# Kernel tuning notes

Measured on AMD Instinct MI355X. Metric: run time of the kernel, lower is better.

The kernel has to match this reference:

```python
import jax, jax.numpy as jnp
import numpy as np

EMBED_DIM = 1536
NUM_HEADS = 12
HEAD_DIM = EMBED_DIM // NUM_HEADS  # 128
SEQ = 2048
EPS = 1e-5


def rms_norm(x, w):
    # x: (..., HEAD_DIM)
    var = jnp.mean(jnp.square(x), axis=-1, keepdims=True)
    return x * jax.lax.rsqrt(var + EPS) * w


def apply_rotary(x, cos, sin):
    # x: (b, s, h, d); cos/sin: (s, d/2) -> broadcast (1, s, 1, d/2)
    d2 = cos.shape[-1]
    c = cos[None, :, None, :]
    s_ = sin[None, :, None, :]
    x1, x2 = x[..., :d2], x[..., d2:]
    return jnp.concatenate([x1 * c - x2 * s_, x2 * c + x1 * s_], axis=-1)


def setup_inputs() -> dict:
    key = jax.random.key(0)
    ks = jax.random.split(key, 10)
    x = jax.random.normal(ks[0], (SEQ, 1, EMBED_DIM), dtype=jnp.float32)
    cu_seqlens = jnp.array([0, SEQ // 2, SEQ], dtype=jnp.int32)
    # rotary tables for positions 0..SEQ-1, rotary dim = HEAD_DIM
    inv_freq = 1.0 / (10000.0 ** (jnp.arange(0, HEAD_DIM, 2, dtype=jnp.float32) / HEAD_DIM))
    pos = jnp.arange(SEQ, dtype=jnp.float32)
    freqs = pos[:, None] * inv_freq[None, :]  # (s, d/2)
    rotary_pos_emb_cos = jnp.cos(freqs)
    rotary_pos_emb_sin = jnp.sin(freqs)
    scale = 0.02
    w_qkv = jax.random.normal(ks[1], (EMBED_DIM, 3 * EMBED_DIM), dtype=jnp.float32) * scale
    b_qkv = jnp.zeros((3 * EMBED_DIM,), dtype=jnp.float32)
    q_norm_w = jnp.ones((HEAD_DIM,), dtype=jnp.float32)
    k_norm_w = jnp.ones((HEAD_DIM,), dtype=jnp.float32)
    w_proj = jax.random.normal(ks[2], (EMBED_DIM, EMBED_DIM), dtype=jnp.float32) * scale
    b_proj = jnp.zeros((EMBED_DIM,), dtype=jnp.float32)
    return {
        'x': x, 'cu_seqlens': cu_seqlens,
        'rotary_pos_emb_cos': rotary_pos_emb_cos, 'rotary_pos_emb_sin': rotary_pos_emb_sin,
        'w_qkv': w_qkv, 'b_qkv': b_qkv, 'q_norm_w': q_norm_w, 'k_norm_w': k_norm_w,
        'w_proj': w_proj, 'b_proj': b_proj,
    }


def reference(x, cu_seqlens, rotary_pos_emb_cos, rotary_pos_emb_sin,
              w_qkv, b_qkv, q_norm_w, k_norm_w, w_proj, b_proj):
    s, b, e = x.shape
    h, d = NUM_HEADS, HEAD_DIM
    qkv = jnp.einsum('sbe,ef->sbf', x, w_qkv) + b_qkv  # (s, b, 3e)
    q, k, v = jnp.split(qkv, 3, axis=2)
    q = q.reshape(s, b, h, d)
    k = k.reshape(s, b, h, d)
    v = v.reshape(s, b, h, d)
    # per-head RMSNorm on q/k
    q = rms_norm(q, q_norm_w)
    k = rms_norm(k, k_norm_w)
    # (s, b, h, d) -> (b, s, h, d)
    q = jnp.transpose(q, (1, 0, 2, 3))
    k = jnp.transpose(k, (1, 0, 2, 3))
    v = jnp.transpose(v, (1, 0, 2, 3))
    q = apply_rotary(q, rotary_pos_emb_cos, rotary_pos_emb_sin)
    k = apply_rotary(k, rotary_pos_emb_cos, rotary_pos_emb_sin)
    # varlen (block-diagonal, non-causal) attention via segment mask
    pos = jnp.arange(s)
    seg = jnp.searchsorted(cu_seqlens[1:], pos, side='right')  # (s,)
    mask = seg[:, None] == seg[None, :]  # (s, s)
    scale = d ** -0.5
    scores = jnp.einsum('bqhd,bkhd->bhqk', q, k) * scale  # (b, h, s, s)
    scores = jnp.where(mask[None, None, :, :], scores, jnp.finfo(scores.dtype).min)
    attn = jax.nn.softmax(scores, axis=-1)
    ctx = jnp.einsum('bhqk,bkhd->bqhd', attn, v)  # (b, s, h, d)
    # (b, s, h, d) -> (s, b, h*d)
    ctx = jnp.transpose(ctx, (1, 0, 2, 3)).reshape(s, b, h * d)
    out = jnp.einsum('sbe,ef->sbf', ctx, w_proj) + b_proj
    return out
```

## Files before the change

kernel.cpp:

```cpp
#include <hip/hip_runtime.h>
#include <hip/hip_bf16.h>
#include <stdint.h>

#define S_LEN 2048
#define EMB   1536
#define NH    12
#define HD    128
#define N3    4608
#define RMS_EPS 1e-5f
#define ATTN_SCALE 0.08838834764831845f
#define SPLIT 3

typedef short short8_t __attribute__((ext_vector_type(8)));
typedef float f32x4    __attribute__((ext_vector_type(4)));

typedef __attribute__((address_space(1))) const void g1_void;
typedef __attribute__((address_space(3))) void l3_void;

__device__ __forceinline__ void gload_lds16(const void* g, void* l) {
  __builtin_amdgcn_global_load_lds((g1_void*)g, (l3_void*)l, 16, 0, 0);
}

__device__ __forceinline__ short f2bf(float f) {
  union { float f; unsigned u; } v; v.f = f;
  unsigned r = (v.u + 0x7FFFu + ((v.u >> 16) & 1u)) >> 16;
  return (short)(r & 0xFFFFu);
}
__device__ __forceinline__ float bf2f(short s) {
  union { unsigned u; float f; } v; v.u = ((unsigned)(unsigned short)s) << 16;
  return v.f;
}

__global__ __launch_bounds__(256) void k_cvt_bf16(const float* __restrict__ in,
                                                  short* __restrict__ out, int n) {
  int i = (blockIdx.x * 256 + threadIdx.x) * 4;
  if (i + 3 < n) {
    float4 v = *(const float4*)(in + i);
    short4 o;
    o.x = f2bf(v.x); o.y = f2bf(v.y); o.z = f2bf(v.z); o.w = f2bf(v.w);
    *(short4*)(out + i) = o;
  }
}

__global__ __launch_bounds__(256) void k_transpose_cvt(const float* __restrict__ W,
                                                       short* __restrict__ Wt,
                                                       int K, int N) {
  __shared__ float t[32][33];
  int n0 = blockIdx.x * 32, k0 = blockIdx.y * 32;
  int tx = threadIdx.x, ty = threadIdx.y;
#pragma unroll
  for (int r = 0; r < 4; ++r) {
    int k = ty + r * 8;
    t[k][tx] = W[(size_t)(k0 + k) * N + n0 + tx];
  }
  __syncthreads();
#pragma unroll
  for (int r = 0; r < 4; ++r) {
    int j = ty + r * 8;
    Wt[(size_t)(n0 + j) * K + k0 + tx] = f2bf(t[tx][j]);
  }
}

template<bool OBF>
__global__ __launch_bounds__(256) void k_gemm_v2(const short* __restrict__ A,
                                                 const short* __restrict__ Bt,
                                                 const float* __restrict__ bias,
                                                 void* __restrict__ Cv,
                                                 int M, int N, int K) {
  __shared__ short lds[2][2][128 * 64];
  const int tid = threadIdx.x;
  const int lane = tid & 63, wid = tid >> 6;
  const int wr = (wid >> 1) * 64, wc = (wid & 1) * 64;
  const int bn = blockIdx.x * 128, bm = blockIdx.y * 128;
  const int lr = lane & 15, lg = lane >> 4;
  const int swz = (lr & 7) << 4;

  const int srow = lane >> 3;
  const int skc  = ((lane & 7) ^ srow) * 8;

  f32x4 acc[4][4] = {};
  const int nk = K >> 6;

#pragma unroll
  for (int it = 0; it < 4; ++it) {
    int seg = wid * 4 + it;
    int row = seg * 8 + srow;
    gload_lds16(A  + (size_t)(bm + row) * K + skc, &lds[0][0][seg * 512]);
    gload_lds16(Bt + (size_t)(bn + row) * K + skc, &lds[0][1][seg * 512]);
  }
  __syncthreads();

  int cur = 0;
  for (int t = 0; t < nk; ++t) {
    if (t + 1 < nk) {
      const int kt = (t + 1) << 6;
#pragma unroll
      for (int it = 0; it < 4; ++it) {
        int seg = wid * 4 + it;
        int row = seg * 8 + srow;
        gload_lds16(A  + (size_t)(bm + row) * K + kt + skc, &lds[cur ^ 1][0][seg * 512]);
        gload_lds16(Bt + (size_t)(bn + row) * K + kt + skc, &lds[cur ^ 1][1][seg * 512]);
      }
    }
    const char* baseA = (const char*)&lds[cur][0][0];
    const char* baseB = (const char*)&lds[cur][1][0];
#pragma unroll
    for (int kk = 0; kk < 2; ++kk) {
      short8_t af[4], bfr[4];
#pragma unroll
      for (int m = 0; m < 4; ++m) {
        int row = wr + m * 16 + lr;
        af[m] = *(const short8_t*)(baseA + ((row * 128 + kk * 64 + lg * 16) ^ swz));
      }
#pragma unroll
      for (int n = 0; n < 4; ++n) {
        int row = wc + n * 16 + lr;
        bfr[n] = *(const short8_t*)(baseB + ((row * 128 + kk * 64 + lg * 16) ^ swz));
      }
#pragma unroll
      for (int m = 0; m < 4; ++m)
#pragma unroll
        for (int n = 0; n < 4; ++n)
          acc[m][n] = __builtin_amdgcn_mfma_f32_16x16x32_bf16(af[m], bfr[n], acc[m][n], 0, 0, 0);
    }
    __syncthreads();
    cur ^= 1;
  }

#pragma unroll
  for (int m = 0; m < 4; ++m)
#pragma unroll
    for (int n = 0; n < 4; ++n) {
      int col = bn + wc + n * 16 + lr;
      float bv = bias[col];
#pragma unroll
      for (int r = 0; r < 4; ++r) {
        int row = bm + wr + m * 16 + lg * 4 + r;
        float v = acc[m][n][r] + bv;
        if (OBF) ((short*)Cv)[(size_t)row * N + col] = f2bf(v);
        else     ((float*)Cv)[(size_t)row * N + col] = v;
      }
    }
}

__global__ __launch_bounds__(256) void k_post(const short* __restrict__ qkv,
                                              const float* __restrict__ cosv,
                                              const float* __restrict__ sinv,
                                              const float* __restrict__ qw,
                                              const float* __restrict__ kw,
                                              short* __restrict__ qb,
                                              short* __restrict__ kb,
                                              short* __restrict__ vt) {
  __shared__ short ldsv[64 * 130];
  const int h = blockIdx.x, s0 = blockIdx.y * 64;
  const int t = threadIdx.x;
  const int r = t >> 2, j = t & 3;
  const int s = s0 + r;
  const size_t rowbase = (size_t)s * N3 + h * HD;

  {
    const short* vp = qkv + rowbase + 2 * EMB + j * 32;
#pragma unroll
    for (int i4 = 0; i4 < 4; ++i4)
      *(short8_t*)&ldsv[r * 130 + j * 32 + i4 * 8] = *(const short8_t*)(vp + i4 * 8);
  }

#pragma unroll
  for (int qk = 0; qk < 2; ++qk) {
    const short* p = qkv + rowbase + qk * EMB + j * 32;
    const float* w = qk ? kw : qw;
    float v[32];
#pragma unroll
    for (int i4 = 0; i4 < 4; ++i4) {
      short8_t x = *(const short8_t*)(p + i4 * 8);
#pragma unroll
      for (int e = 0; e < 8; ++e) v[i4 * 8 + e] = bf2f(x[e]);
    }
    float ss = 0.f;
#pragma unroll
    for (int i = 0; i < 32; ++i) ss += v[i] * v[i];
    ss += __shfl_xor(ss, 1);
    ss += __shfl_xor(ss, 2);
    float rsq = rsqrtf(ss * (1.0f / HD) + RMS_EPS);
#pragma unroll
    for (int i = 0; i < 32; ++i) v[i] = v[i] * rsq * w[j * 32 + i];
    const float* cp = cosv + (size_t)s * 64 + (j & 1) * 32;
    const float* sp = sinv + (size_t)s * 64 + (j & 1) * 32;
    short out[32];
#pragma unroll
    for (int i = 0; i < 32; ++i) {
      float part = __shfl_xor(v[i], 2);
      float c = cp[i], sn = sp[i];
      float o = (j < 2) ? (v[i] * c - part * sn) : (v[i] * c + part * sn);
      out[i] = f2bf(o);
    }
    short* dst = (qk ? kb : qb) + ((size_t)h * S_LEN + s) * HD + j * 32;
#pragma unroll
    for (int i4 = 0; i4 < 4; ++i4) {
      short8_t o8;
#pragma unroll
      for (int e = 0; e < 8; ++e) o8[e] = out[i4 * 8 + e];
      *(short8_t*)(dst + i4 * 8) = o8;
    }
  }

  __syncthreads();
  const int sl = t & 63, wv = t >> 6;
#pragma unroll
  for (int it = 0; it < 32; ++it) {
    int d = it * 4 + wv;
    vt[((size_t)h * HD + d) * S_LEN + s0 + sl] = ldsv[sl * 130 + d];
  }
}

__global__ __launch_bounds__(256) void k_attn(const short* __restrict__ qb,
                                              const short* __restrict__ kb,
                                              const short* __restrict__ vt,
                                              const int* __restrict__ cu, int nseg,
                                              short* __restrict__ Opart,
                                              float* __restrict__ mlpart) {
  __shared__ short ldsK[64 * 128];
  __shared__ short ldsV[128 * 64];
  __shared__ short ldsP[4 * 16 * 64];

  const int h = blockIdx.x, qt = blockIdx.y, p = blockIdx.z;
  const int q0 = qt * 64;
  const int tid = threadIdx.x, l = tid & 63, w = tid >> 6;
  const int lr = l & 15, lg = l >> 4;

  int rs[4], re[4];
  float m[4], lsum[4];
#pragma unroll
  for (int r = 0; r < 4; ++r) {
    int row = q0 + w * 16 + lg * 4 + r;
    int seg = 0;
    for (int i = 1; i <= nseg; ++i) if (row >= cu[i]) seg = i;
    rs[r] = (seg == 0) ? 0 : cu[seg];
    re[r] = (seg < nseg) ? cu[seg + 1] : S_LEN;
    m[r] = -INFINITY;
    lsum[r] = 0.f;
  }

  int seg0 = 0, seg1 = 0;
  for (int i = 1; i <= nseg; ++i) {
    if (q0 >= cu[i]) seg0 = i;
    if (q0 + 63 >= cu[i]) seg1 = i;
  }
  const int ks = (seg0 == 0) ? 0 : cu[seg0];
  const int ke = (seg1 < nseg) ? cu[seg1 + 1] : S_LEN;
  const int kt0 = (ks >> 6) << 6;
  const int nt = (ke - kt0 + 63) >> 6;
  const int tpb = (nt + SPLIT - 1) / SPLIT;
  const int tb0 = p * tpb;
  const int tb1 = (tb0 + tpb < nt) ? tb0 + tpb : nt;

  short8_t qf[4];
  {
    int srow = q0 + w * 16 + lr;
    const short* qp = qb + ((size_t)h * S_LEN + srow) * HD;
#pragma unroll
    for (int kk = 0; kk < 4; ++kk)
      qf[kk] = *(const short8_t*)(qp + kk * 32 + lg * 8);
  }

  f32x4 cacc[8] = {};

  for (int ti = tb0; ti < tb1; ++ti) {
    const int kt = kt0 + ti * 64;
    __syncthreads();
#pragma unroll
    for (int it = 0; it < 4; ++it) {
      int c = it * 256 + tid;
      int row = c >> 4, cc = c & 15;
      short8_t v = *(const short8_t*)&kb[((size_t)h * S_LEN + kt + row) * HD + cc * 8];
      int byte = row * 256 + cc * 16;
      byte ^= (row & 7) << 4;
      *(short8_t*)((char*)ldsK + byte) = v;
    }
#pragma unroll
    for (int it = 0; it < 4; ++it) {
      int c = it * 256 + tid;
      int d = c >> 3, cc = c & 7;
      short8_t v = *(const short8_t*)&vt[((size_t)h * HD + d) * S_LEN + kt + cc * 8];
      int byte = d * 128 + cc * 16;
      byte ^= (d & 7) << 4;
      *(short8_t*)((char*)ldsV + byte) = v;
    }
    __syncthreads();

    f32x4 sacc[4] = {};
#pragma unroll
    for (int n = 0; n < 4; ++n) {
#pragma unroll
      for (int kk = 0; kk < 4; ++kk) {
        int row = n * 16 + lr;
        int byte = row * 256 + (kk * 32 + lg * 8) * 2;
        byte ^= (row & 7) << 4;
        short8_t kf = *(const short8_t*)((const char*)ldsK + byte);
        sacc[n] = __builtin_amdgcn_mfma_f32_16x16x32_bf16(qf[kk], kf, sacc[n], 0, 0, 0);
      }
    }

    float sv[4][4];
#pragma unroll
    for (int n = 0; n < 4; ++n) {
      int key = kt + n * 16 + lr;
#pragma unroll
      for (int r = 0; r < 4; ++r) {
        float x = sacc[n][r] * ATTN_SCALE;
        sv[n][r] = (key >= rs[r] && key < re[r]) ? x : -1e30f;
      }
    }
    float alpha[4];
#pragma unroll
    for (int r = 0; r < 4; ++r) {
      float tm = fmaxf(fmaxf(sv[0][r], sv[1][r]), fmaxf(sv[2][r], sv[3][r]));
#pragma unroll
      for (int off = 1; off < 16; off <<= 1) tm = fmaxf(tm, __shfl_xor(tm, off));
      float mn = fmaxf(m[r], tm);
      alpha[r] = __expf(m[r] - mn);
      m[r] = mn;
      float ls = 0.f;
#pragma unroll
      for (int n = 0; n < 4; ++n) {
        float pv = __expf(sv[n][r] - mn);
        sv[n][r] = pv;
        ls += pv;
      }
#pragma unroll
      for (int off = 1; off < 16; off <<= 1) ls += __shfl_xor(ls, off);
      lsum[r] = lsum[r] * alpha[r] + ls;
    }
#pragma unroll
    for (int n = 0; n < 8; ++n)
#pragma unroll
      for (int r = 0; r < 4; ++r) cacc[n][r] *= alpha[r];

#pragma unroll
    for (int n = 0; n < 4; ++n)
#pragma unroll
      for (int r = 0; r < 4; ++r) {
        int prow = lg * 4 + r;
        int pcol = n * 16 + lr;
        int byte = prow * 128 + pcol * 2;
        byte ^= (prow & 7) << 4;
        *(short*)((char*)ldsP + w * 2048 + byte) = f2bf(sv[n][r]);
      }
    __syncthreads();

#pragma unroll
    for (int kk = 0; kk < 2; ++kk) {
      int byteP = lr * 128 + (kk * 32 + lg * 8) * 2;
      byteP ^= (lr & 7) << 4;
      short8_t pf = *(const short8_t*)((const char*)ldsP + w * 2048 + byteP);
#pragma unroll
      for (int n = 0; n < 8; ++n) {
        int d = n * 16 + lr;
        int byteV = d * 128 + (kk * 32 + lg * 8) * 2;
        byteV ^= (d & 7) << 4;
        short8_t vf = *(const short8_t*)((const char*)ldsV + byteV);
        cacc[n] = __builtin_amdgcn_mfma_f32_16x16x32_bf16(pf, vf, cacc[n], 0, 0, 0);
      }
    }
  }

  const int b = (h * 32 + qt) * SPLIT + p;
#pragma unroll
  for (int r = 0; r < 4; ++r) {
    int qrow = w * 16 + lg * 4 + r;
#pragma unroll
    for (int n = 0; n < 8; ++n)
      Opart[(size_t)b * 8192 + qrow * 128 + n * 16 + lr] = f2bf(cacc[n][r]);
  }
  if (lr == 0) {
#pragma unroll
    for (int r = 0; r < 4; ++r) {
      int qrow = w * 16 + lg * 4 + r;
      mlpart[(size_t)b * 128 + qrow] = m[r];
      mlpart[(size_t)b * 128 + 64 + qrow] = lsum[r];
    }
  }
}

__global__ __launch_bounds__(256) void k_combine(const short* __restrict__ Opart,
                                                 const float* __restrict__ ml,
                                                 short* __restrict__ ctx) {
  const int h = blockIdx.x, qt = blockIdx.y, t = threadIdx.x;
  const int r = t >> 2, j = t & 3;
  const int b0 = (h * 32 + qt) * SPLIT;

  float mp[SPLIT], lp[SPLIT], wp[SPLIT];
  float M = -INFINITY;
#pragma unroll
  for (int p = 0; p < SPLIT; ++p) {
    mp[p] = ml[(size_t)(b0 + p) * 128 + r];
    lp[p] = ml[(size_t)(b0 + p) * 128 + 64 + r];
    M = fmaxf(M, mp[p]);
  }
  float L = 0.f;
#pragma unroll
  for (int p = 0; p < SPLIT; ++p) {
    wp[p] = __expf(mp[p] - M);
    L += lp[p] * wp[p];
  }
  const float inv = 1.0f / L;

  float acc[32];
#pragma unroll
  for (int i = 0; i < 32; ++i) acc[i] = 0.f;
#pragma unroll
  for (int p = 0; p < SPLIT; ++p) {
    const short* src = Opart + (size_t)(b0 + p) * 8192 + r * 128 + j * 32;
#pragma unroll
    for (int i4 = 0; i4 < 4; ++i4) {
      short8_t v = *(const short8_t*)(src + i4 * 8);
#pragma unroll
      for (int e = 0; e < 8; ++e) acc[i4 * 8 + e] += wp[p] * bf2f(v[e]);
    }
  }

  short* dst = ctx + (size_t)(qt * 64 + r) * EMB + h * HD + j * 32;
#pragma unroll
  for (int i4 = 0; i4 < 4; ++i4) {
    short8_t o8;
#pragma unroll
    for (int e = 0; e < 8; ++e) o8[e] = f2bf(acc[i4 * 8 + e] * inv);
    *(short8_t*)(dst + i4 * 8) = o8;
  }
}

extern "C" void kernel_launch(void* const* d_in, const int* in_sizes, int n_in,
                              void* d_out, int out_size, void* d_ws, size_t ws_size,
                              hipStream_t stream) {
  const float* x      = (const float*)d_in[0];
  const int*   cu     = (const int*)d_in[1];
  const float* cosv   = (const float*)d_in[2];
  const float* sinv   = (const float*)d_in[3];
  const float* w_qkv  = (const float*)d_in[4];
  const float* b_qkv  = (const float*)d_in[5];
  const float* q_norm = (const float*)d_in[6];
  const float* k_norm = (const float*)d_in[7];
  const float* w_proj = (const float*)d_in[8];
  const float* b_proj = (const float*)d_in[9];
  const int nseg = in_sizes[1] - 1;

  char* ws = (char*)d_ws;
  short* xb     = (short*)(ws);
  short* wqkvT  = (short*)(ws + 6291456);
  short* wprojT = (short*)(ws + 20447232);
  short* qkv16  = (short*)(ws + 25165824);
  short* qb     = (short*)(ws + 44040192);
  short* kb     = (short*)(ws + 50331648);
  short* vt     = (short*)(ws + 56623104);
  short* ctxb   = (short*)(ws + 62914560);
  short* Opart  = qkv16;
  float* mlpart = (float*)ws;

  k_cvt_bf16<<<(S_LEN * EMB) / 1024, 256, 0, stream>>>(x, xb, S_LEN * EMB);
  k_transpose_cvt<<<dim3(N3 / 32, EMB / 32), dim3(32, 8), 0, stream>>>(w_qkv, wqkvT, EMB, N3);
  k_transpose_cvt<<<dim3(EMB / 32, EMB / 32), dim3(32, 8), 0, stream>>>(w_proj, wprojT, EMB, EMB);
  k_gemm_v2<true><<<dim3(N3 / 128, S_LEN / 128), 256, 0, stream>>>(xb, wqkvT, b_qkv, qkv16, S_LEN, N3, EMB);
  k_post<<<dim3(NH, S_LEN / 64), 256, 0, stream>>>(qkv16, cosv, sinv, q_norm, k_norm, qb, kb, vt);
  k_attn<<<dim3(NH, S_LEN / 64, SPLIT), 256, 0, stream>>>(qb, kb, vt, cu, nseg, Opart, mlpart);
  k_combine<<<dim3(NH, S_LEN / 64), 256, 0, stream>>>(Opart, mlpart, ctxb);
  k_gemm_v2<false><<<dim3(EMB / 128, S_LEN / 128), 256, 0, stream>>>(ctxb, wprojT, b_proj, (float*)d_out, S_LEN, EMB, EMB);
}
```

Baseline: 153.0 us.

## Double-buffer K/V with async global-to-LDS loads and 128-row query tiles

The attention kernel now uses 512 threads covering 128 query rows per block, so each K/V tile is reused by twice as many query rows. K and V tiles are prefetched with direct global-to-LDS loads into a double buffer, letting the next tile's load overlap with the current tile's compute. One barrier per iteration is dropped and the split-K factor falls from 3 to 2, with the combine kernel updated to match. This cuts the grid size, which may lower parallelism, and the sync between prefetch issue and consumption relies on the end-of-iteration barrier to make the async loads visible.

Measured after the change: 183.3 us. 1.2x slower.

```diff
diff --git a/kernel.cpp b/kernel.cpp
--- a/kernel.cpp
+++ b/kernel.cpp
@@ -9,7 +9,7 @@
 #define N3    4608
 #define RMS_EPS 1e-5f
 #define ATTN_SCALE 0.08838834764831845f
-#define SPLIT 3
+#define SPLIT 2
 
 typedef short short8_t __attribute__((ext_vector_type(8)));
 typedef float f32x4    __attribute__((ext_vector_type(4)));
@@ -213,20 +213,23 @@
   }
 }
 
-__global__ __launch_bounds__(256) void k_attn(const short* __restrict__ qb,
-                                              const short* __restrict__ kb,
-                                              const short* __restrict__ vt,
-                                              const int* __restrict__ cu, int nseg,
-                                              short* __restrict__ Opart,
-                                              float* __restrict__ mlpart) {
-  __shared__ short ldsK[64 * 128];
-  __shared__ short ldsV[128 * 64];
-  __shared__ short ldsP[4 * 16 * 64];
+__global__ __launch_bounds__(512, 4) void k_attn(const short* __restrict__ qb,
+                                                 const short* __restrict__ kb,
+                                                 const short* __restrict__ vt,
+                                                 const int* __restrict__ cu, int nseg,
+                                                 short* __restrict__ Opart,
+                                                 float* __restrict__ mlpart) {
+  __shared__ short ldsK[2][64 * 128];
+  __shared__ short ldsV[2][128 * 64];
+  __shared__ short ldsP[8 * 16 * 64];
 
   const int h = blockIdx.x, qt = blockIdx.y, p = blockIdx.z;
-  const int q0 = qt * 64;
+  const int q0 = qt * 128;
   const int tid = threadIdx.x, l = tid & 63, w = tid >> 6;
   const int lr = l & 15, lg = l >> 4;
+
+  const short* kb_h = kb + (size_t)h * S_LEN * HD;
+  const short* vt_h = vt + (size_t)h * HD * S_LEN;
 
   int rs[4], re[4];
   float m[4], lsum[4];
@@ -244,7 +247,7 @@
   int seg0 = 0, seg1 = 0;
   for (int i = 1; i <= nseg; ++i) {
     if (q0 >= cu[i]) seg0 = i;
-    if (q0 + 63 >= cu[i]) seg1 = i;
+    if (q0 + 127 >= cu[i]) seg1 = i;
   }
   const int ks = (seg0 == 0) ? 0 : cu[seg0];
   const int ke = (seg1 < nseg) ? cu[seg1 + 1] : S_LEN;
@@ -254,6 +257,9 @@
   const int tb0 = p * tpb;
   const int tb1 = (tb0 + tpb < nt) ? tb0 + tpb : nt;
 
+  const int kseg_row = l >> 4;
+  const int vseg_row = l >> 3;
+
   short8_t qf[4];
   {
     int srow = q0 + w * 16 + lr;
@@ -265,28 +271,40 @@
 
   f32x4 cacc[8] = {};
 
+  if (tb0 < tb1) {
+    const int kt = kt0 + tb0 * 64;
+#pragma unroll
+    for (int it = 0; it < 2; ++it) {
+      int s = w * 2 + it;
+      int lrow = s * 4 + kseg_row;
+      int sck = ((l & 15) ^ (lrow & 7)) * 8;
+      gload_lds16(kb_h + (size_t)(kt + lrow) * HD + sck, &ldsK[0][s * 512]);
+      int drow = s * 8 + vseg_row;
+      int scv = ((l & 7) ^ (drow & 7)) * 8;
+      gload_lds16(vt_h + (size_t)drow * S_LEN + kt + scv, &ldsV[0][s * 512]);
+    }
+  }
+  __syncthreads();
+
+  int cur = 0;
   for (int ti = tb0; ti < tb1; ++ti) {
     const int kt = kt0 + ti * 64;
-    __syncthreads();
-#pragma unroll
-    for (int it = 0; it < 4; ++it) {
-      int c = it * 256 + tid;
-      int row = c >> 4, cc = c & 15;
-      short8_t v = *(const short8_t*)&kb[((size_t)h * S_LEN + kt + row) * HD + cc * 8];
-      int byte = row * 256 + cc * 16;
-      byte ^= (row & 7) << 4;
-      *(short8_t*)((char*)ldsK + byte) = v;
-    }
-#pragma unroll
-    for (int it = 0; it < 4; ++it) {
-      int c = it * 256 + tid;
-      int d = c >> 3, cc = c & 7;
-      short8_t v = *(const short8_t*)&vt[((size_t)h * HD + d) * S_LEN + kt + cc * 8];
-      int byte = d * 128 + cc * 16;
-      byte ^= (d & 7) << 4;
-      *(short8_t*)((char*)ldsV + byte) = v;
-    }
-    __syncthreads();
+    if (ti + 1 < tb1) {
+      const int ktn = kt + 64;
+#pragma unroll
+      for (int it = 0; it < 2; ++it) {
+        int s = w * 2 + it;
+        int lrow = s * 4 + kseg_row;
+        int sck = ((l & 15) ^ (lrow & 7)) * 8;
+        gload_lds16(kb_h + (size_t)(ktn + lrow) * HD + sck, &ldsK[cur ^ 1][s * 512]);
+        int drow = s * 8 + vseg_row;
+        int scv = ((l & 7) ^ (drow & 7)) * 8;
+        gload_lds16(vt_h + (size_t)drow * S_LEN + ktn + scv, &ldsV[cur ^ 1][s * 512]);
+      }
+    }
+
+    const char* bK = (const char*)&ldsK[cur][0];
+    const char* bV = (const char*)&ldsV[cur][0];
 
     f32x4 sacc[4] = {};
 #pragma unroll
@@ -296,7 +314,7 @@
         int row = n * 16 + lr;
         int byte = row * 256 + (kk * 32 + lg * 8) * 2;
         byte ^= (row & 7) << 4;
-        short8_t kf = *(const short8_t*)((const char*)ldsK + byte);
+        short8_t kf = *(const short8_t*)(bK + byte);
         sacc[n] = __builtin_amdgcn_mfma_f32_16x16x32_bf16(qf[kk], kf, sacc[n], 0, 0, 0);
       }
     }
@@ -346,7 +364,6 @@
         byte ^= (prow & 7) << 4;
         *(short*)((char*)ldsP + w * 2048 + byte) = f2bf(sv[n][r]);
       }
-    __syncthreads();
 
 #pragma unroll
     for (int kk = 0; kk < 2; ++kk) {
@@ -358,43 +375,46 @@
         int d = n * 16 + lr;
         int byteV = d * 128 + (kk * 32 + lg * 8) * 2;
         byteV ^= (d & 7) << 4;
-        short8_t vf = *(const short8_t*)((const char*)ldsV + byteV);
+        short8_t vf = *(const short8_t*)(bV + byteV);
         cacc[n] = __builtin_amdgcn_mfma_f32_16x16x32_bf16(pf, vf, cacc[n], 0, 0, 0);
       }
     }
-  }
-
-  const int b = (h * 32 + qt) * SPLIT + p;
+
+    __syncthreads();
+    cur ^= 1;
+  }
+
+  const int b = (h * 16 + qt) * SPLIT + p;
 #pragma unroll
   for (int r = 0; r < 4; ++r) {
     int qrow = w * 16 + lg * 4 + r;
 #pragma unroll
     for (int n = 0; n < 8; ++n)
-      Opart[(size_t)b * 8192 + qrow * 128 + n * 16 + lr] = f2bf(cacc[n][r]);
+      Opart[(size_t)b * 16384 + qrow * 128 + n * 16 + lr] = f2bf(cacc[n][r]);
   }
   if (lr == 0) {
 #pragma unroll
     for (int r = 0; r < 4; ++r) {
       int qrow = w * 16 + lg * 4 + r;
-      mlpart[(size_t)b * 128 + qrow] = m[r];
-      mlpart[(size_t)b * 128 + 64 + qrow] = lsum[r];
-    }
-  }
-}
-
-__global__ __launch_bounds__(256) void k_combine(const short* __restrict__ Opart,
+      mlpart[(size_t)b * 256 + qrow] = m[r];
+      mlpart[(size_t)b * 256 + 128 + qrow] = lsum[r];
+    }
+  }
+}
+
+__global__ __launch_bounds__(512) void k_combine(const short* __restrict__ Opart,
                                                  const float* __restrict__ ml,
                                                  short* __restrict__ ctx) {
   const int h = blockIdx.x, qt = blockIdx.y, t = threadIdx.x;
   const int r = t >> 2, j = t & 3;
-  const int b0 = (h * 32 + qt) * SPLIT;
+  const int b0 = (h * 16 + qt) * SPLIT;
 
   float mp[SPLIT], lp[SPLIT], wp[SPLIT];
   float M = -INFINITY;
 #pragma unroll
   for (int p = 0; p < SPLIT; ++p) {
-    mp[p] = ml[(size_t)(b0 + p) * 128 + r];
-    lp[p] = ml[(size_t)(b0 + p) * 128 + 64 + r];
+    mp[p] = ml[(size_t)(b0 + p) * 256 + r];
+    lp[p] = ml[(size_t)(b0 + p) * 256 + 128 + r];
     M = fmaxf(M, mp[p]);
   }
   float L = 0.f;
@@ -410,7 +430,7 @@
   for (int i = 0; i < 32; ++i) acc[i] = 0.f;
 #pragma unroll
   for (int p = 0; p < SPLIT; ++p) {
-    const short* src = Opart + (size_t)(b0 + p) * 8192 + r * 128 + j * 32;
+    const short* src = Opart + (size_t)(b0 + p) * 16384 + r * 128 + j * 32;
 #pragma unroll
     for (int i4 = 0; i4 < 4; ++i4) {
       short8_t v = *(const short8_t*)(src + i4 * 8);
@@ -419,7 +439,7 @@
     }
   }
 
-  short* dst = ctx + (size_t)(qt * 64 + r) * EMB + h * HD + j * 32;
+  short* dst = ctx + (size_t)(qt * 128 + r) * EMB + h * HD + j * 32;
 #pragma unroll
   for (int i4 = 0; i4 < 4; ++i4) {
     short8_t o8;
@@ -461,7 +481,7 @@
   k_transpose_cvt<<<dim3(EMB / 32, EMB / 32), dim3(32, 8), 0, stream>>>(w_proj, wprojT, EMB, EMB);
   k_gemm_v2<true><<<dim3(N3 / 128, S_LEN / 128), 256, 0, stream>>>(xb, wqkvT, b_qkv, qkv16, S_LEN, N3, EMB);
   k_post<<<dim3(NH, S_LEN / 64), 256, 0, stream>>>(qkv16, cosv, sinv, q_norm, k_norm, qb, kb, vt);
-  k_attn<<<dim3(NH, S_LEN / 64, SPLIT), 256, 0, stream>>>(qb, kb, vt, cu, nseg, Opart, mlpart);
-  k_combine<<<dim3(NH, S_LEN / 64), 256, 0, stream>>>(Opart, mlpart, ctxb);
+  k_attn<<<dim3(NH, S_LEN / 128, SPLIT), 512, 0, stream>>>(qb, kb, vt, cu, nseg, Opart, mlpart);
+  k_combine<<<dim3(NH, S_LEN / 128), 512, 0, stream>>>(Opart, mlpart, ctxb);
   k_gemm_v2<false><<<dim3(EMB / 128, S_LEN / 128), 256, 0, stream>>>(ctxb, wprojT, b_proj, (float*)d_out, S_LEN, EMB, EMB);
 }
```
